# Performance work log

Measured on AMD Instinct MI355X. Metric: run time of the kernel, lower is better.

The kernel has to match this reference:

```python
import jax, jax.numpy as jnp
import numpy as np

NUM_HEADS = 32
HEAD_DIM = 512
EPS = 1e-12  # torch F.normalize eps


def setup_inputs() -> dict:
    key = jax.random.key(0)
    k1, k2, k3, k4, k5 = jax.random.split(key, 5)
    B, C, H, W = 32, 256, 64, 64
    return {
        "X": jax.random.normal(k1, (B, C, H, W), dtype=jnp.float32),
        "qkv_w": jax.random.normal(k2, (3 * HEAD_DIM, C), dtype=jnp.float32) * 0.02,
        "qkv_b": jax.random.normal(k3, (3 * HEAD_DIM,), dtype=jnp.float32) * 0.02,
        "proj_w": jax.random.normal(k4, (C, HEAD_DIM), dtype=jnp.float32) * 0.02,
        "proj_b": jax.random.normal(k5, (C,), dtype=jnp.float32) * 0.02,
    }


def _l2norm_axis1(x):
    # torch F.normalize(x, dim=1): x / max(||x||_2, eps)
    n = jnp.sqrt(jnp.sum(x * x, axis=1, keepdims=True))
    return x / jnp.maximum(n, EPS)


def reference(X, qkv_w, qkv_b, proj_w, proj_b):
    B, C, H, W = X.shape
    # 1x1 conv == channel matmul: [B,3*hd,H,W]
    qkv = jnp.einsum('bchw,oc->bohw', X, qkv_w) + qkv_b[None, :, None, None]
    # reshape to (B, 3, num_heads, head_dim, L) where L = H*W // num_heads
    qkv = qkv.reshape(B, 3, NUM_HEADS, HEAD_DIM, -1)
    q, k, v = qkv[:, 0], qkv[:, 1], qkv[:, 2]  # [B, nh, hd, L]
    # normalize across the num_heads axis (dim=1), as in the original code
    q = _l2norm_axis1(q)
    k = _l2norm_axis1(k)
    # attn = q^T @ k : [B, nh, L, L]
    attn = jnp.einsum('bhdl,bhdm->bhlm', q, k)
    attn = jax.nn.softmax(attn, axis=-1)
    # output = v @ attn^T : [B, nh, hd, L]
    out = jnp.einsum('bhdm,bhlm->bhdl', v, attn)
    out = out.reshape(B, HEAD_DIM, H, W)
    # proj 1x1 conv back to C channels
    out = jnp.einsum('bdhw,cd->bchw', out, proj_w) + proj_b[None, :, None, None]
    return out
```

## Files before the change

### kernel.cpp

```cpp
#include <hip/hip_runtime.h>
#include <stdint.h>


typedef float     f32x4   __attribute__((ext_vector_type(4)));
typedef short     bf16x8  __attribute__((ext_vector_type(8)));
typedef float     floatx4 __attribute__((ext_vector_type(4)));
typedef uint16_t  ushortx8 __attribute__((ext_vector_type(8)));
typedef uint16_t  ushortx4 __attribute__((ext_vector_type(4)));

#define DEVI static __device__ __forceinline__

DEVI float bf2f(uint16_t u) { union { uint32_t i; float f; } x; x.i = ((uint32_t)u) << 16; return x.f; }
DEVI uint16_t f2bf(float f) {
  union { float f; uint32_t i; } x; x.f = f;
  uint32_t r = x.i + 0x7fff + ((x.i >> 16) & 1);
  return (uint16_t)(r >> 16);
}

DEVI void gload16(const void* g, void* l) {
  __builtin_amdgcn_global_load_lds((const __attribute__((address_space(1))) void*)g,
                                   (__attribute__((address_space(3))) void*)l, 16, 0, 0);
}

DEVI float redmax16(float v) {
  v = fmaxf(v, __shfl_xor(v, 1)); v = fmaxf(v, __shfl_xor(v, 2));
  v = fmaxf(v, __shfl_xor(v, 4)); v = fmaxf(v, __shfl_xor(v, 8));
  return v;
}
DEVI float redsum16(float v) {
  v += __shfl_xor(v, 1); v += __shfl_xor(v, 2);
  v += __shfl_xor(v, 4); v += __shfl_xor(v, 8);
  return v;
}

__global__ __launch_bounds__(256) void k_transpose_x(const float* __restrict__ X,
                                                     uint16_t* __restrict__ Xt) {
  __shared__ float tile[64][65];
  int t = threadIdx.x;
  int st = blockIdx.x, ct = blockIdx.y, b = blockIdx.z;
  int row = t >> 2, cq = t & 3;
  const float* src = X + ((size_t)(b * 256 + ct * 64 + row)) * 4096 + st * 64 + cq * 16;
#pragma unroll
  for (int k = 0; k < 4; ++k) {
    floatx4 v = *(const floatx4*)(src + k * 4);
    tile[row][cq * 16 + k * 4 + 0] = v[0];
    tile[row][cq * 16 + k * 4 + 1] = v[1];
    tile[row][cq * 16 + k * 4 + 2] = v[2];
    tile[row][cq * 16 + k * 4 + 3] = v[3];
  }
  __syncthreads();
  int srow = t >> 2, oq = t & 3;
  ushortx8 o0, o1;
#pragma unroll
  for (int k = 0; k < 8; ++k) o0[k] = f2bf(tile[oq * 16 + k][srow]);
#pragma unroll
  for (int k = 0; k < 8; ++k) o1[k] = f2bf(tile[oq * 16 + 8 + k][srow]);
  uint16_t* dst = Xt + ((size_t)(b * 4096 + st * 64 + srow)) * 256 + ct * 64 + oq * 16;
  *(ushortx8*)dst = o0;
  *(ushortx8*)(dst + 8) = o1;
}

__global__ __launch_bounds__(256) void k_cvt_bf16(const float* __restrict__ src,
                                                  uint16_t* __restrict__ dst, int n) {
  int i = (blockIdx.x * 256 + threadIdx.x) * 4;
  if (i >= n) return;
  floatx4 v = *(const floatx4*)(src + i);
  ushortx4 o;
  o[0] = f2bf(v[0]); o[1] = f2bf(v[1]); o[2] = f2bf(v[2]); o[3] = f2bf(v[3]);
  *(ushortx4*)(dst + i) = o;
}

__global__ __launch_bounds__(256) void k_qkv_gemm(const uint16_t* __restrict__ W,
                                                  const uint16_t* __restrict__ Xt,
                                                  const float* __restrict__ bias_g,
                                                  uint16_t* __restrict__ qkv) {
  __shared__ __align__(16) uint16_t As[128 * 64];
  __shared__ __align__(16) uint16_t Bs[128 * 64];
  int t = threadIdx.x, lane = t & 63, wave = t >> 6;
  int st = blockIdx.x, ot = blockIdx.y, b = blockIdx.z;
  int wr = wave >> 1, wc = wave & 1;
  f32x4 acc[4][4] = {};
  int srow = lane >> 3;
  int sc_us = ((((lane & 7) * 16) ^ ((srow & 7) << 4)) >> 1);
  const uint16_t* Ag = W + (size_t)(ot * 128 + wave * 8 + srow) * 256;
  const uint16_t* Bg = Xt + ((size_t)(b * 4096 + st * 128 + wave * 8 + srow)) * 256;

  for (int kc = 0; kc < 4; ++kc) {
    __syncthreads();
#pragma unroll
    for (int c = 0; c < 4; ++c) {
      gload16(Ag + (size_t)(c * 32) * 256 + kc * 64 + sc_us, &As[(c * 32 + wave * 8) * 64]);
      gload16(Bg + (size_t)(c * 32) * 256 + kc * 64 + sc_us, &Bs[(c * 32 + wave * 8) * 64]);
    }
    __syncthreads();
#pragma unroll
    for (int kk = 0; kk < 2; ++kk) {
      bf16x8 a[4], bw[4];
#pragma unroll
      for (int i = 0; i < 4; ++i) {
        int r = wr * 64 + i * 16 + (lane & 15);
        a[i] = *(const bf16x8*)&As[r * 64 + ((kk * 32 + (lane >> 4) * 8) ^ ((r & 7) << 3))];
      }
#pragma unroll
      for (int j = 0; j < 4; ++j) {
        int r = wc * 64 + j * 16 + (lane & 15);
        bw[j] = *(const bf16x8*)&Bs[r * 64 + ((kk * 32 + (lane >> 4) * 8) ^ ((r & 7) << 3))];
      }
#pragma unroll
      for (int i = 0; i < 4; ++i)
#pragma unroll
        for (int j = 0; j < 4; ++j)
          acc[i][j] = __builtin_amdgcn_mfma_f32_16x16x32_bf16(a[i], bw[j], acc[i][j], 0, 0, 0);
    }
  }
  int o0 = ot * 128 + wr * 64, s0 = st * 128 + wc * 64;
  float bv[4][4];
#pragma unroll
  for (int i = 0; i < 4; ++i)
#pragma unroll
    for (int r = 0; r < 4; ++r) bv[i][r] = bias_g[o0 + i * 16 + (lane >> 4) * 4 + r];
#pragma unroll
  for (int i = 0; i < 4; ++i)
#pragma unroll
    for (int j = 0; j < 4; ++j)
#pragma unroll
      for (int r = 0; r < 4; ++r) {
        int o = o0 + i * 16 + (lane >> 4) * 4 + r;
        int s = s0 + j * 16 + (lane & 15);
        qkv[((size_t)b * 1536 + o) * 4096 + s] = f2bf(acc[i][j][r] + bv[i][r]);
      }
}

__global__ __launch_bounds__(256) void k_reformat(const uint16_t* __restrict__ qkv,
                                                  uint16_t* __restrict__ Qp,
                                                  uint16_t* __restrict__ Kp) {
  __shared__ float scale_lds[16 * 520];
  __shared__ __align__(16) uint16_t data_lds[16 * 520];
  int t = threadIdx.x;
  int shc = blockIdx.x, g = blockIdx.y, b = blockIdx.z;
  int s0 = shc * 512;
  const uint16_t* base = qkv + ((size_t)(b * 1536 + g * 512)) * 4096;
  uint16_t* dst = (g ? Kp : Qp) + (size_t)b * 32 * 65536;

  float ss[4][8] = {};
  for (int h = 0; h < 32; ++h) {
#pragma unroll
    for (int sl = 0; sl < 4; ++sl) {
      int id = sl * 256 + t, c16 = id >> 6, oc = id & 63;
      ushortx8 v = *(const ushortx8*)(base + ((size_t)(h * 16 + c16)) * 4096 + s0 + oc * 8);
#pragma unroll
      for (int j = 0; j < 8; ++j) { float f = bf2f(v[j]); ss[sl][j] += f * f; }
    }
  }
#pragma unroll
  for (int sl = 0; sl < 4; ++sl) {
    int id = sl * 256 + t, c16 = id >> 6, oc = id & 63;
#pragma unroll
    for (int j = 0; j < 8; ++j) {
      float n = sqrtf(ss[sl][j]);
      scale_lds[c16 * 520 + oc * 8 + j] = 1.0f / fmaxf(n, 1e-12f);
    }
  }
  __syncthreads();

  for (int h = 0; h < 32; ++h) {
#pragma unroll
    for (int sl = 0; sl < 4; ++sl) {
      int id = sl * 256 + t, c16 = id >> 6, oc = id & 63;
      ushortx8 v = *(const ushortx8*)(base + ((size_t)(h * 16 + c16)) * 4096 + s0 + oc * 8);
      *(ushortx8*)&data_lds[c16 * 520 + oc * 8] = v;
    }
    __syncthreads();
    uint16_t* drow = dst + (size_t)h * 65536 + shc * 64;
#pragma unroll
    for (int i = 0; i < 4; ++i) {
      int id = i * 256 + t, l = id >> 3, od = id & 7;
      ushortx8 o8;
#pragma unroll
      for (int jj = 0; jj < 8; ++jj) {
        int dpr = od * 8 + jj, shr = dpr >> 4, c16 = dpr & 15;
        int idx = c16 * 520 + shr * 128 + l;
        o8[jj] = f2bf(bf2f(data_lds[idx]) * scale_lds[idx]);
      }
      *(ushortx8*)(drow + (size_t)l * 512 + od * 8) = o8;
    }
    __syncthreads();
  }
}

__global__ __launch_bounds__(256) void k_attn(const uint16_t* __restrict__ Qp,
                                              const uint16_t* __restrict__ Kp,
                                              const uint16_t* qkv,
                                              uint16_t* OtBase) {
  __shared__ __align__(16) uint16_t smemA[16384];
  __shared__ __align__(16) uint16_t Pb[16384];
  __shared__ float rsum[128];
  int t = threadIdx.x, lane = t & 63, w = t >> 6;
  int h = blockIdx.x, b = blockIdx.y;
  const size_t bh = (size_t)(b * 32 + h);
  const uint16_t* Qg = Qp + bh * 65536;
  const uint16_t* Kg = Kp + bh * 65536;
  uint16_t* QT = smemA;
  uint16_t* KT = smemA + 8192;
  int srow = lane >> 3;
  int sc_us = ((((lane & 7) * 16) ^ ((srow & 7) << 4)) >> 1);

  f32x4 accs[2][8] = {};
  for (int kc = 0; kc < 8; ++kc) {
    __syncthreads();
#pragma unroll
    for (int c = 0; c < 4; ++c) {
      int r = c * 32 + w * 8 + srow;
      gload16(Qg + (size_t)r * 512 + kc * 64 + sc_us, &QT[(c * 32 + w * 8) * 64]);
      gload16(Kg + (size_t)r * 512 + kc * 64 + sc_us, &KT[(c * 32 + w * 8) * 64]);
    }
    __syncthreads();
#pragma unroll
    for (int kk = 0; kk < 2; ++kk) {
      bf16x8 aq[2];
#pragma unroll
      for (int lf = 0; lf < 2; ++lf) {
        int r = w * 32 + lf * 16 + (lane & 15);
        aq[lf] = *(const bf16x8*)&QT[r * 64 + ((kk * 32 + (lane >> 4) * 8) ^ ((r & 7) << 3))];
      }
#pragma unroll
      for (int mf = 0; mf < 8; ++mf) {
        int r = mf * 16 + (lane & 15);
        bf16x8 bk = *(const bf16x8*)&KT[r * 64 + ((kk * 32 + (lane >> 4) * 8) ^ ((r & 7) << 3))];
        accs[0][mf] = __builtin_amdgcn_mfma_f32_16x16x32_bf16(aq[0], bk, accs[0][mf], 0, 0, 0);
        accs[1][mf] = __builtin_amdgcn_mfma_f32_16x16x32_bf16(aq[1], bk, accs[1][mf], 0, 0, 0);
      }
    }
  }

#pragma unroll
  for (int lf = 0; lf < 2; ++lf) {
#pragma unroll
    for (int r = 0; r < 4; ++r) {
      float mx = accs[lf][0][r];
#pragma unroll
      for (int mf = 1; mf < 8; ++mf) mx = fmaxf(mx, accs[lf][mf][r]);
      mx = redmax16(mx);
      float sum = 0.f;
#pragma unroll
      for (int mf = 0; mf < 8; ++mf) {
        float e = __expf(accs[lf][mf][r] - mx);
        accs[lf][mf][r] = e;
        sum += e;
      }
      sum = redsum16(sum);
      int l = w * 32 + lf * 16 + (lane >> 4) * 4 + r;
      if ((lane & 15) == 0) rsum[l] = 1.0f / sum;
#pragma unroll
      for (int mf = 0; mf < 8; ++mf) {
        int m = mf * 16 + (lane & 15);
        Pb[l * 128 + (m ^ ((l & 7) << 3))] = f2bf(accs[lf][mf][r]);
      }
    }
  }
  __syncthreads();

  uint16_t* Vt = smemA;
  const uint16_t* vg = qkv + ((size_t)(b * 1536 + 1024 + h * 16)) * 4096;
  int vrow = lane >> 2;
  int vcol_us = ((((lane & 3) * 16) ^ ((vrow & 3) << 4)) >> 1);
  uint16_t* OtB = OtBase + (size_t)b * 6291456;

#pragma unroll
  for (int lc = 0; lc < 2; ++lc) {
    f32x4 acco[8][4] = {};
    for (int mc = 0; mc < 4; ++mc) {
      __syncthreads();
#pragma unroll
      for (int c = 0; c < 8; ++c) {
        int d = c * 64 + w * 16 + vrow;
        gload16(vg + (size_t)(d >> 5) * 4096 + (d & 31) * 128 + mc * 32 + vcol_us,
                &Vt[(c * 64 + w * 16) * 32]);
      }
      __syncthreads();
      bf16x8 av[8], bp[4];
#pragma unroll
      for (int df = 0; df < 8; ++df) {
        int r = w * 128 + df * 16 + (lane & 15);
        av[df] = *(const bf16x8*)&Vt[r * 32 + (((lane >> 4) * 8) ^ ((r & 3) << 3))];
      }
#pragma unroll
      for (int lf = 0; lf < 4; ++lf) {
        int l = lc * 64 + lf * 16 + (lane & 15);
        bp[lf] = *(const bf16x8*)&Pb[l * 128 + ((mc * 32 + (lane >> 4) * 8) ^ ((l & 7) << 3))];
      }
#pragma unroll
      for (int df = 0; df < 8; ++df)
#pragma unroll
        for (int lf = 0; lf < 4; ++lf)
          acco[df][lf] = __builtin_amdgcn_mfma_f32_16x16x32_bf16(av[df], bp[lf], acco[df][lf], 0, 0, 0);
    }
    float scl[4];
#pragma unroll
    for (int lf = 0; lf < 4; ++lf) scl[lf] = rsum[lc * 64 + lf * 16 + (lane & 15)];

#pragma unroll
    for (int half = 0; half < 2; ++half) {
      __syncthreads();
#pragma unroll
      for (int df = 0; df < 8; ++df)
#pragma unroll
        for (int lf2 = 0; lf2 < 2; ++lf2) {
          int lf = half * 2 + lf2;
          int lloc = lf2 * 16 + (lane & 15);
#pragma unroll
          for (int r = 0; r < 4; ++r) {
            int d = w * 128 + df * 16 + (lane >> 4) * 4 + r;
            Vt[(lloc * 32 + (d & 31)) * 16 + (d >> 5)] = f2bf(acco[df][lf][r] * scl[lf]);
          }
        }
      __syncthreads();
#pragma unroll
      for (int i = 0; i < 4; ++i) {
        int chunk = i * 256 + t;
        int lloc = chunk >> 5, dlo = chunk & 31;
        int l = lc * 64 + half * 32 + lloc;
        ushortx8 v0 = *(ushortx8*)&Vt[chunk * 16];
        ushortx8 v1 = *(ushortx8*)&Vt[chunk * 16 + 8];
        uint16_t* gp = OtB + ((size_t)(dlo * 128 + l)) * 512 + h * 16;
        *(ushortx8*)gp = v0;
        *(ushortx8*)(gp + 8) = v1;
      }
    }
  }
}

__global__ __launch_bounds__(256) void k_proj_gemm(const uint16_t* __restrict__ Wp,
                                                   const uint16_t* __restrict__ Ot,
                                                   const float* __restrict__ bias_g,
                                                   float* __restrict__ outp) {
  __shared__ __align__(16) uint16_t As[128 * 64];
  __shared__ __align__(16) uint16_t Bs[128 * 64];
  int t = threadIdx.x, lane = t & 63, wave = t >> 6;
  int st = blockIdx.x, ct = blockIdx.y, b = blockIdx.z;
  int wr = wave >> 1, wc = wave & 1;
  f32x4 acc[4][4] = {};
  int srow = lane >> 3;
  int sc_us = ((((lane & 7) * 16) ^ ((srow & 7) << 4)) >> 1);
  const uint16_t* Ag = Wp + (size_t)(ct * 128 + wave * 8 + srow) * 512;
  const uint16_t* Bg = Ot + (size_t)b * 6291456 + ((size_t)(st * 128 + wave * 8 + srow)) * 512;

  for (int kc = 0; kc < 8; ++kc) {
    __syncthreads();
#pragma unroll
    for (int c = 0; c < 4; ++c) {
      gload16(Ag + (size_t)(c * 32) * 512 + kc * 64 + sc_us, &As[(c * 32 + wave * 8) * 64]);
      gload16(Bg + (size_t)(c * 32) * 512 + kc * 64 + sc_us, &Bs[(c * 32 + wave * 8) * 64]);
    }
    __syncthreads();
#pragma unroll
    for (int kk = 0; kk < 2; ++kk) {
      bf16x8 a[4], bw[4];
#pragma unroll
      for (int i = 0; i < 4; ++i) {
        int r = wr * 64 + i * 16 + (lane & 15);
        a[i] = *(const bf16x8*)&As[r * 64 + ((kk * 32 + (lane >> 4) * 8) ^ ((r & 7) << 3))];
      }
#pragma unroll
      for (int j = 0; j < 4; ++j) {
        int r = wc * 64 + j * 16 + (lane & 15);
        bw[j] = *(const bf16x8*)&Bs[r * 64 + ((kk * 32 + (lane >> 4) * 8) ^ ((r & 7) << 3))];
      }
#pragma unroll
      for (int i = 0; i < 4; ++i)
#pragma unroll
        for (int j = 0; j < 4; ++j)
          acc[i][j] = __builtin_amdgcn_mfma_f32_16x16x32_bf16(a[i], bw[j], acc[i][j], 0, 0, 0);
    }
  }
  int c0 = ct * 128 + wr * 64, s0 = st * 128 + wc * 64;
  float bv[4][4];
#pragma unroll
  for (int i = 0; i < 4; ++i)
#pragma unroll
    for (int r = 0; r < 4; ++r) bv[i][r] = bias_g[c0 + i * 16 + (lane >> 4) * 4 + r];
#pragma unroll
  for (int i = 0; i < 4; ++i)
#pragma unroll
    for (int j = 0; j < 4; ++j)
#pragma unroll
      for (int r = 0; r < 4; ++r) {
        int c = c0 + i * 16 + (lane >> 4) * 4 + r;
        int s = s0 + j * 16 + (lane & 15);
        outp[((size_t)b * 256 + c) * 4096 + s] = acc[i][j][r] + bv[i][r];
      }
}

extern "C" void kernel_launch(void* const* d_in, const int* in_sizes, int n_in,
                              void* d_out, int out_size, void* d_ws, size_t ws_size,
                              hipStream_t stream) {
  const float* X      = (const float*)d_in[0];
  const float* qkv_w  = (const float*)d_in[1];
  const float* qkv_b  = (const float*)d_in[2];
  const float* proj_w = (const float*)d_in[3];
  const float* proj_b = (const float*)d_in[4];
  float* outp = (float*)d_out;

  const size_t SZ_XT  = 2097152;
  const size_t SZ_QKV = 12582912;
  const size_t SZ_QP  = 4194304;
  const size_t SZ_W   = 786432 + 262144;

  int NB = 0;
  const int cand[6] = {32, 16, 8, 4, 2, 1};
  for (int ci = 0; ci < 6; ++ci) {
    size_t need = SZ_W + (size_t)cand[ci] * (SZ_XT + SZ_QKV + 2 * SZ_QP);
    if (need <= ws_size) { NB = cand[ci]; break; }
  }
  if (NB == 0) return;

  char* ws = (char*)d_ws;
  uint16_t* Wqb  = (uint16_t*)(ws);
  uint16_t* Wpb  = (uint16_t*)(ws + 786432);
  char*     gbuf = ws + SZ_W;
  uint16_t* Xt   = (uint16_t*)(gbuf);
  uint16_t* qkvb = (uint16_t*)(gbuf + (size_t)NB * SZ_XT);
  uint16_t* Qp   = (uint16_t*)(gbuf + (size_t)NB * (SZ_XT + SZ_QKV));
  uint16_t* Kp   = (uint16_t*)(gbuf + (size_t)NB * (SZ_XT + SZ_QKV + SZ_QP));

  k_cvt_bf16<<<dim3(384), 256, 0, stream>>>(qkv_w, Wqb, 1536 * 256);
  k_cvt_bf16<<<dim3(128), 256, 0, stream>>>(proj_w, Wpb, 256 * 512);

  for (int b0 = 0; b0 < 32; b0 += NB) {
    const float* Xg   = X + (size_t)b0 * 256 * 4096;
    float*       outg = outp + (size_t)b0 * 256 * 4096;
    k_transpose_x<<<dim3(64, 4, NB), 256, 0, stream>>>(Xg, Xt);
    k_qkv_gemm<<<dim3(32, 12, NB), 256, 0, stream>>>(Wqb, Xt, qkv_b, qkvb);
    k_reformat<<<dim3(8, 2, NB), 256, 0, stream>>>(qkvb, Qp, Kp);
    k_attn<<<dim3(32, NB), 256, 0, stream>>>(Qp, Kp, qkvb, qkvb );
    k_proj_gemm<<<dim3(32, 2, NB), 256, 0, stream>>>(Wpb, qkvb , proj_b, outg);
  }
}
```

Before: 686.0 us.

## Split reformat into scale-computation and apply kernels for more parallelism

The single reformat kernel, which ran only 8x2xNB blocks that each looped over all heads, is replaced by two kernels. One computes the inverse L2 norms across heads into a float scratch buffer that reuses the Xt workspace. The other, launched with 8x32x2NB blocks, applies the scales and writes the transposed Q/K layouts. This raises occupancy for a memory-bound step that was launch-starved. In exchange it adds a second pass over qkv, a scale buffer round trip through global memory, and uncoalesced scalar gathers in the apply kernel.

```diff
diff --git a/kernel.cpp b/kernel.cpp
--- a/kernel.cpp
+++ b/kernel.cpp
@@ -131,60 +131,53 @@
       }
 }
 
-__global__ __launch_bounds__(256) void k_reformat(const uint16_t* __restrict__ qkv,
-                                                  uint16_t* __restrict__ Qp,
-                                                  uint16_t* __restrict__ Kp) {
-  __shared__ float scale_lds[16 * 520];
-  __shared__ __align__(16) uint16_t data_lds[16 * 520];
+__global__ __launch_bounds__(256) void k_scales(const uint16_t* __restrict__ qkv,
+                                                float* __restrict__ scaleB) {
   int t = threadIdx.x;
-  int shc = blockIdx.x, g = blockIdx.y, b = blockIdx.z;
-  int s0 = shc * 512;
+  int sc = blockIdx.x, g = blockIdx.y, b = blockIdx.z;
   const uint16_t* base = qkv + ((size_t)(b * 1536 + g * 512)) * 4096;
-  uint16_t* dst = (g ? Kp : Qp) + (size_t)b * 32 * 65536;
-
-  float ss[4][8] = {};
+  float* sb = scaleB + ((size_t)(b * 2 + g)) * 16 * 4096;
+  int c16 = t >> 4, so = t & 15;
+  int s = sc * 128 + so * 8;
+  float ss[8] = {};
   for (int h = 0; h < 32; ++h) {
-#pragma unroll
-    for (int sl = 0; sl < 4; ++sl) {
-      int id = sl * 256 + t, c16 = id >> 6, oc = id & 63;
-      ushortx8 v = *(const ushortx8*)(base + ((size_t)(h * 16 + c16)) * 4096 + s0 + oc * 8);
-#pragma unroll
-      for (int j = 0; j < 8; ++j) { float f = bf2f(v[j]); ss[sl][j] += f * f; }
-    }
-  }
-#pragma unroll
-  for (int sl = 0; sl < 4; ++sl) {
-    int id = sl * 256 + t, c16 = id >> 6, oc = id & 63;
-#pragma unroll
-    for (int j = 0; j < 8; ++j) {
-      float n = sqrtf(ss[sl][j]);
-      scale_lds[c16 * 520 + oc * 8 + j] = 1.0f / fmaxf(n, 1e-12f);
-    }
-  }
-  __syncthreads();
-
-  for (int h = 0; h < 32; ++h) {
-#pragma unroll
-    for (int sl = 0; sl < 4; ++sl) {
-      int id = sl * 256 + t, c16 = id >> 6, oc = id & 63;
-      ushortx8 v = *(const ushortx8*)(base + ((size_t)(h * 16 + c16)) * 4096 + s0 + oc * 8);
-      *(ushortx8*)&data_lds[c16 * 520 + oc * 8] = v;
-    }
-    __syncthreads();
-    uint16_t* drow = dst + (size_t)h * 65536 + shc * 64;
-#pragma unroll
-    for (int i = 0; i < 4; ++i) {
-      int id = i * 256 + t, l = id >> 3, od = id & 7;
-      ushortx8 o8;
-#pragma unroll
-      for (int jj = 0; jj < 8; ++jj) {
-        int dpr = od * 8 + jj, shr = dpr >> 4, c16 = dpr & 15;
-        int idx = c16 * 520 + shr * 128 + l;
-        o8[jj] = f2bf(bf2f(data_lds[idx]) * scale_lds[idx]);
-      }
-      *(ushortx8*)(drow + (size_t)l * 512 + od * 8) = o8;
-    }
-    __syncthreads();
+    ushortx8 v = *(const ushortx8*)(base + ((size_t)(h * 16 + c16)) * 4096 + s);
+#pragma unroll
+    for (int j = 0; j < 8; ++j) { float f = bf2f(v[j]); ss[j] += f * f; }
+  }
+  floatx4 o0, o1;
+#pragma unroll
+  for (int j = 0; j < 4; ++j) o0[j] = 1.0f / fmaxf(sqrtf(ss[j]), 1e-12f);
+#pragma unroll
+  for (int j = 0; j < 4; ++j) o1[j] = 1.0f / fmaxf(sqrtf(ss[4 + j]), 1e-12f);
+  *(floatx4*)(sb + c16 * 4096 + s) = o0;
+  *(floatx4*)(sb + c16 * 4096 + s + 4) = o1;
+}
+
+__global__ __launch_bounds__(256) void k_apply(const uint16_t* __restrict__ qkv,
+                                               const float* __restrict__ scaleB,
+                                               uint16_t* __restrict__ Qp,
+                                               uint16_t* __restrict__ Kp) {
+  int t = threadIdx.x;
+  int shc = blockIdx.x, h = blockIdx.y, z = blockIdx.z;
+  int b = z >> 1, g = z & 1;
+  const uint16_t* base = qkv + ((size_t)(b * 1536 + g * 512 + h * 16)) * 4096;
+  const float* sb = scaleB + ((size_t)(b * 2 + g)) * 16 * 4096;
+  uint16_t* dst = (g ? Kp : Qp) + (size_t)b * 32 * 65536 + (size_t)h * 65536;
+#pragma unroll
+  for (int k = 0; k < 4; ++k) {
+    int id = k * 256 + t;
+    int l = id & 127, od = id >> 7;
+    ushortx8 o;
+#pragma unroll
+    for (int jj = 0; jj < 8; ++jj) {
+      int dp = od * 8 + jj;
+      int c16 = dp & 15;
+      int s = (shc * 4 + (dp >> 4)) * 128 + l;
+      float v = bf2f(base[(size_t)c16 * 4096 + s]);
+      o[jj] = f2bf(v * sb[c16 * 4096 + s]);
+    }
+    *(ushortx8*)(dst + (size_t)l * 512 + shc * 64 + od * 8) = o;
   }
 }
 
@@ -422,6 +415,7 @@
   uint16_t* qkvb = (uint16_t*)(gbuf + (size_t)NB * SZ_XT);
   uint16_t* Qp   = (uint16_t*)(gbuf + (size_t)NB * (SZ_XT + SZ_QKV));
   uint16_t* Kp   = (uint16_t*)(gbuf + (size_t)NB * (SZ_XT + SZ_QKV + SZ_QP));
+  float*    scaleB = (float*)Xt;
 
   k_cvt_bf16<<<dim3(384), 256, 0, stream>>>(qkv_w, Wqb, 1536 * 256);
   k_cvt_bf16<<<dim3(128), 256, 0, stream>>>(proj_w, Wpb, 256 * 512);
@@ -431,7 +425,8 @@
     float*       outg = outp + (size_t)b0 * 256 * 4096;
     k_transpose_x<<<dim3(64, 4, NB), 256, 0, stream>>>(Xg, Xt);
     k_qkv_gemm<<<dim3(32, 12, NB), 256, 0, stream>>>(Wqb, Xt, qkv_b, qkvb);
-    k_reformat<<<dim3(8, 2, NB), 256, 0, stream>>>(qkvb, Qp, Kp);
+    k_scales<<<dim3(32, 2, NB), 256, 0, stream>>>(qkvb, scaleB);
+    k_apply<<<dim3(8, 32, 2 * NB), 256, 0, stream>>>(qkvb, scaleB, Qp, Kp);
     k_attn<<<dim3(32, NB), 256, 0, stream>>>(Qp, Kp, qkvb, qkvb );
     k_proj_gemm<<<dim3(32, 2, NB), 256, 0, stream>>>(Wpb, qkvb , proj_b, outg);
   }
```

Measured after the change: 671.0 us. 1.02x faster.
